# Kernel optimization log

Hardware: AMD Instinct MI355X
Metric: run time of the kernel (lower is better)

## Reference

```python
import jax, jax.numpy as jnp
import numpy as np

B, N, M, G = 2, 8192, 8192, 256
X_MIN = Y_MIN = -35.0
CELL = abs(2.0 * X_MIN / G)  # cell size, as in construct_batched_cuda_grid


def setup_inputs() -> dict:
    key = jax.random.key(0)
    k1, k2, k3, k4, k5 = jax.random.split(key, 5)
    p_i = jax.random.uniform(k1, (B, N, 3), jnp.float32, -34.0, 34.0)
    p_j = jax.random.uniform(k2, (B, M, 3), jnp.float32, -34.0, 34.0)
    mos = jax.random.normal(k3, (B, 2, G, G), jnp.float32)
    error_p_i_flow = jax.random.uniform(k4, (B, N), jnp.float32)
    nearest_flow = jax.random.randint(k5, (B, N, 1), 0, M, jnp.int32)
    return {"p_i": p_i, "mos": mos, "p_j": p_j,
            "error_p_i_flow": error_p_i_flow, "nearest_flow": nearest_flow}


def _knn1_l1(x, y):
    # brute-force 1-NN with L1 (norm=1) distance, matching knn_points(..., K=1, norm=1)
    # build (B,N,M) dist one coordinate at a time to avoid a (B,N,M,3) intermediate
    d = (jnp.abs(x[:, :, None, 0] - y[:, None, :, 0])
         + jnp.abs(x[:, :, None, 1] - y[:, None, :, 1])
         + jnp.abs(x[:, :, None, 2] - y[:, None, :, 2]))
    return jnp.min(d, axis=-1), jnp.argmin(d, axis=-1)


def reference(p_i, mos, p_j, error_p_i_flow, nearest_flow):
    # NN_loss with reduction='none' -> error_p_i_rigid = (cham_x + cham_y)/2 (needs N==M)
    cham_x, nearest_rigid = _knn1_l1(p_i, p_j)  # (B,N), (B,N)
    cham_y, _ = _knn1_l1(p_j, p_i)              # (B,M)
    error_p_i_rigid = (cham_x + cham_y) * 0.5

    dynamic = error_p_i_flow > error_p_i_rigid             # (B,N) bool
    idx = jnp.where(dynamic, nearest_flow[..., 0], nearest_rigid)  # (B,N)
    art_labels = dynamic.astype(jnp.int32)                 # (B,N) in {0,1}

    # batched gather p_j[b, idx[b]]
    p_j_by_nn = jnp.take_along_axis(p_j, idx[..., None], axis=1)  # (B,N,3)

    # construct_batched_cuda_grid: scatter labels into (B,G,G), -1 elsewhere
    shift = jnp.array([X_MIN, Y_MIN], jnp.float32)
    cell_idx = ((p_j_by_nn[:, :, :2] - shift) / CELL).astype(jnp.int32)  # (B,N,2)
    bs = jnp.repeat(jnp.arange(B), N)
    grid = -jnp.ones((B, G, G), jnp.int32)
    grid = grid.at[bs,
                   cell_idx[..., 0].reshape(-1),
                   cell_idx[..., 1].reshape(-1)].set(art_labels.reshape(-1))

    # CrossEntropyLoss(ignore_index=-1), mean over non-ignored cells
    logp = jax.nn.log_softmax(mos, axis=1)                 # (B,C,G,G)
    valid = grid >= 0
    tgt = jnp.clip(grid, 0, None)
    lp = jnp.take_along_axis(logp, tgt[:, None], axis=1)[:, 0]  # (B,G,G)
    loss = -jnp.where(valid, lp, 0.0).sum() / jnp.maximum(valid.sum(), 1).astype(lp.dtype)
    return loss
```

## Files before the change

kernel.cpp:

```cpp
#include <hip/hip_runtime.h>
#include <float.h>

#define B_ 2
#define N_ 8192
#define G_ 256
constexpr float X_MIN_F = -35.0f;
constexpr float CELL_F  = 0.2734375f;

using u64 = unsigned long long;

#define OFF_ACCUM 524288
#define OFF_PX    524352

template<int CC>
__global__ __launch_bounds__(256) void nn_kernel(const float* __restrict__ p_i,
                                                 const float* __restrict__ p_j,
                                                 u64* __restrict__ px,
                                                 float* __restrict__ colpart,
                                                 int* __restrict__ grid,
                                                 unsigned* __restrict__ accum)
{
    constexpr int COLS = N_ / CC;
    const int b    = blockIdx.z;
    const int tid  = threadIdx.x;
    const int lane = tid & 63;
    const int w    = tid >> 6;
    const int row0 = blockIdx.x * 2048 + tid * 8;
    const int c0   = blockIdx.y * COLS;

    __shared__ __align__(16) float q[COLS * 3];
    __shared__ __align__(16) float sc[4][8][36];
    __shared__ float colW[4][COLS];

    const float* __restrict__ Qg = p_j + ((size_t)b * N_ + c0) * 3;
    for (int t = tid; t < COLS * 3 / 4; t += 256)
        ((float4*)q)[t] = ((const float4*)Qg)[t];

    {
        const int lin = blockIdx.x + 4 * (blockIdx.y + CC * blockIdx.z);
        constexpr int NB  = 8 * CC;
        constexpr int PER = 32768 / NB;
        for (int t = tid; t < PER; t += 256)
            ((uint4*)grid)[lin * PER + t] = make_uint4(~0u, ~0u, ~0u, ~0u);
        if (lin == 0 && tid < 4) accum[tid] = 0u;
    }

    const float4* pp = (const float4*)(p_i + ((size_t)b * N_ + row0) * 3);
    float4 a0 = pp[0], a1 = pp[1], a2 = pp[2];
    float4 a3 = pp[3], a4 = pp[4], a5 = pp[5];
    float px_[8] = {a0.x, a0.w, a1.z, a2.y, a3.x, a3.w, a4.z, a5.y};
    float py_[8] = {a0.y, a1.x, a1.w, a2.z, a3.y, a4.x, a4.w, a5.z};
    float pz_[8] = {a0.z, a1.y, a2.x, a2.w, a3.z, a4.y, a5.x, a5.w};

    float best[8];
    int   gcol[8];
#pragma unroll
    for (int r = 0; r < 8; r++) { best[r] = FLT_MAX; gcol[r] = 0; }

    __syncthreads();

    for (int jg = 0; jg < COLS; jg += 8) {
        const float4* qv = (const float4*)&q[jg * 3];
        float4 v0 = qv[0], v1 = qv[1], v2 = qv[2];
        float4 v3 = qv[3], v4 = qv[4], v5 = qv[5];
        float qx[8] = {v0.x, v0.w, v1.z, v2.y, v3.x, v3.w, v4.z, v5.y};
        float qy[8] = {v0.y, v1.x, v1.w, v2.z, v3.y, v4.x, v4.w, v5.z};
        float qz[8] = {v0.z, v1.y, v2.x, v2.w, v3.z, v4.y, v5.x, v5.w};

        float part[8];
        {
            float dm[4][8];
#pragma unroll
            for (int r = 0; r < 4; r++) {
#pragma unroll
                for (int k = 0; k < 8; k++)
                    dm[r][k] = (fabsf(px_[r] - qx[k]) + fabsf(py_[r] - qy[k]))
                               + fabsf(pz_[r] - qz[k]);
                float m = fminf(fminf(dm[r][0], dm[r][1]), dm[r][2]);
                m = fminf(fminf(m, dm[r][3]), dm[r][4]);
                m = fminf(fminf(m, dm[r][5]), dm[r][6]);
                m = fminf(m, dm[r][7]);
                bool lt = m < best[r];
                best[r] = lt ? m : best[r];
                gcol[r] = lt ? jg : gcol[r];
            }
#pragma unroll
            for (int k = 0; k < 8; k++)
                part[k] = fminf(fminf(fminf(dm[0][k], dm[1][k]), dm[2][k]),
                                dm[3][k]);
        }
        {
            float dm[4][8];
#pragma unroll
            for (int r = 0; r < 4; r++) {
                const int rr = r + 4;
#pragma unroll
                for (int k = 0; k < 8; k++)
                    dm[r][k] = (fabsf(px_[rr] - qx[k]) + fabsf(py_[rr] - qy[k]))
                               + fabsf(pz_[rr] - qz[k]);
                float m = fminf(fminf(dm[r][0], dm[r][1]), dm[r][2]);
                m = fminf(fminf(m, dm[r][3]), dm[r][4]);
                m = fminf(fminf(m, dm[r][5]), dm[r][6]);
                m = fminf(m, dm[r][7]);
                bool lt = m < best[rr];
                best[rr] = lt ? m : best[rr];
                gcol[rr] = lt ? jg : gcol[rr];
            }
#pragma unroll
            for (int k = 0; k < 8; k++)
                part[k] = fminf(part[k],
                                fminf(fminf(fminf(dm[0][k], dm[1][k]),
                                            dm[2][k]), dm[3][k]));
        }

#pragma unroll
        for (int k = 0; k < 8; k++) {
            unsigned a = __float_as_uint(part[k]);
            auto pr = __builtin_amdgcn_permlane32_swap(a, a, false, false);
            part[k] = fminf(__uint_as_float(pr[0]), __uint_as_float(pr[1]));
        }
#pragma unroll
        for (int k = 0; k < 8; k++)
            sc[w][k][lane & 31] = part[k];
        const int kc = lane >> 3, mc = lane & 7;
        float4 c4v = *(const float4*)&sc[w][kc][4 * mc];
        float c4 = fminf(fminf(c4v.x, c4v.y), fminf(c4v.z, c4v.w));
        c4 = fminf(c4, __shfl_xor(c4, 1));
        c4 = fminf(c4, __shfl_xor(c4, 2));
        c4 = fminf(c4, __shfl_xor(c4, 4));
        if (mc == 0) colW[w][jg + kc] = c4;
    }

    __syncthreads();

    for (int t = tid; t < COLS; t += 256) {
        float c = fminf(fminf(colW[0][t], colW[1][t]),
                        fminf(colW[2][t], colW[3][t]));
        colpart[(size_t)blockIdx.x * (B_ * N_) + (size_t)b * N_ + c0 + t] = c;
    }

    int bidx[8];
#pragma unroll
    for (int r = 0; r < 8; r++) {
        const float4* qv = (const float4*)&q[gcol[r] * 3];
        float4 v0 = qv[0], v1 = qv[1], v2 = qv[2];
        float4 v3 = qv[3], v4 = qv[4], v5 = qv[5];
        float qx[8] = {v0.x, v0.w, v1.z, v2.y, v3.x, v3.w, v4.z, v5.y};
        float qy[8] = {v0.y, v1.x, v1.w, v2.z, v3.y, v4.x, v4.w, v5.z};
        float qz[8] = {v0.z, v1.y, v2.x, v2.w, v3.z, v4.y, v5.x, v5.w};
        int kk = 0;
#pragma unroll
        for (int k = 7; k >= 0; k--) {
            float d = (fabsf(px_[r] - qx[k]) + fabsf(py_[r] - qy[k]))
                      + fabsf(pz_[r] - qz[k]);
            kk = (d == best[r]) ? k : kk;
        }
        bidx[r] = c0 + gcol[r] + kk;
    }
    const size_t o = (size_t)blockIdx.y * (B_ * N_) + b * N_ + row0;
#pragma unroll
    for (int r = 0; r < 8; r++)
        px[o + r] = ((u64)__float_as_uint(best[r]) << 32) | (unsigned)bidx[r];
}

template<int CC>
__global__ __launch_bounds__(256) void reduce_scatter_kernel(
    const u64* __restrict__ px, const float* __restrict__ cp,
    const float* __restrict__ flow, const int* __restrict__ nflow,
    const float* __restrict__ Pj, int* __restrict__ grid)
{
    __shared__ u64      sbx[64];
    __shared__ unsigned sby[64];
    const int tid = threadIdx.x;
    const int p   = tid & 63;
    const int g   = tid >> 6;
    constexpr int CPG = CC / 4;

    if (tid < 64) { sbx[tid] = ~0ull; sby[tid] = ~0u; }
    __syncthreads();

    const int pt = blockIdx.x * 64 + p;
    u64 bx = ~0ull;
#pragma unroll
    for (int k = 0; k < CPG; k++) {
        int c = g * CPG + k;
        u64 v = px[(size_t)c * (B_ * N_) + pt];
        bx = v < bx ? v : bx;
    }
    float by = cp[(size_t)g * (B_ * N_) + pt];
    atomicMin(&sbx[p], bx);
    atomicMin(&sby[p], __float_as_uint(by));
    __syncthreads();

    if (tid < 64) {
        u64 fx = sbx[tid];
        float dx = __uint_as_float((unsigned)(fx >> 32));
        float dy = __uint_as_float(sby[tid]);
        float rigid = (dx + dy) * 0.5f;

        const int i = blockIdx.x * 64 + tid;
        const int b = i >> 13;
        const int n = i & (N_ - 1);

        bool dyn  = flow[i] > rigid;
        int label = dyn ? 1 : 0;
        int idx   = dyn ? nflow[i] : (int)(unsigned)(fx & 0xFFFFFFFFull);

        const float* qp = Pj + ((size_t)b * N_ + idx) * 3;
        float xx = qp[0], yy = qp[1];

        int cx = (int)((xx - X_MIN_F) / CELL_F);
        int cy = (int)((yy - X_MIN_F) / CELL_F);

        atomicMax(&grid[(b << 16) + cx * G_ + cy], (n << 1) | label);
    }
}

__global__ __launch_bounds__(256) void ce_kernel(const float* __restrict__ mos,
                                                 const int* __restrict__ grid,
                                                 float* __restrict__ accum,
                                                 float* __restrict__ out)
{
    int i = blockIdx.x * 256 + threadIdx.x;
    float lsum = 0.0f;
    int   lcnt = 0;

    int packed = grid[i];
    if (packed >= 0) {
        int b    = i >> 16;
        int cell = i & 0xFFFF;
        float m0 = mos[((size_t)b * 2 + 0) * 65536 + cell];
        float m1 = mos[((size_t)b * 2 + 1) * 65536 + cell];
        float mx = fmaxf(m0, m1);
        float lse = logf(expf(m0 - mx) + expf(m1 - mx));
        float sh  = ((packed & 1) ? m1 : m0) - mx;
        lsum = sh - lse;
        lcnt = 1;
    }

#pragma unroll
    for (int o = 32; o > 0; o >>= 1) {
        lsum += __shfl_down(lsum, o);
        lcnt += __shfl_down(lcnt, o);
    }
    __shared__ float wsum[4];
    __shared__ int   wcnt[4];
    int wave = threadIdx.x >> 6;
    if ((threadIdx.x & 63) == 0) { wsum[wave] = lsum; wcnt[wave] = lcnt; }
    __syncthreads();
    if (threadIdx.x == 0) {
        float s = wsum[0] + wsum[1] + wsum[2] + wsum[3];
        int   c = wcnt[0] + wcnt[1] + wcnt[2] + wcnt[3];
        atomicAdd(&accum[0], s);
        atomicAdd((int*)&accum[1], c);
        __threadfence();
        unsigned t = atomicAdd((unsigned*)&accum[2], 1u);
        if (t == gridDim.x - 1) {
            float S = atomicAdd(&accum[0], 0.0f);
            int   C = atomicAdd((int*)&accum[1], 0);
            out[0] = -S / (float)(C > 0 ? C : 1);
        }
    }
}

template<int CC>
static void run(const float* p_i, const float* mos, const float* p_j,
                const float* flow, const int* nflow, float* out,
                char* ws, hipStream_t stream)
{
    int*   grid    = (int*)ws;
    float* accum   = (float*)(ws + OFF_ACCUM);
    u64*   px      = (u64*)(ws + OFF_PX);
    float* colpart = (float*)(ws + OFF_PX + (size_t)CC * B_ * N_ * 8);

    dim3 g(4, CC, 2);
    nn_kernel<CC><<<g, 256, 0, stream>>>(p_i, p_j, px, colpart, (int*)grid,
                                         (unsigned*)accum);
    reduce_scatter_kernel<CC><<<256, 256, 0, stream>>>(px, colpart, flow,
                                                       nflow, p_j, grid);
    ce_kernel<<<(B_ * G_ * G_) / 256, 256, 0, stream>>>(mos, grid, accum, out);
}

extern "C" void kernel_launch(void* const* d_in, const int* in_sizes, int n_in,
                              void* d_out, int out_size, void* d_ws, size_t ws_size,
                              hipStream_t stream)
{
    const float* p_i   = (const float*)d_in[0];
    const float* mos   = (const float*)d_in[1];
    const float* p_j   = (const float*)d_in[2];
    const float* flow  = (const float*)d_in[3];
    const int*   nflow = (const int*)d_in[4];
    float* out = (float*)d_out;
    char* ws = (char*)d_ws;

    constexpr size_t CPART = (size_t)4 * B_ * N_ * 4;
    if (ws_size >= OFF_PX + (size_t)64 * B_ * N_ * 8 + CPART)
        run<64>(p_i, mos, p_j, flow, nflow, out, ws, stream);
    else if (ws_size >= OFF_PX + (size_t)16 * B_ * N_ * 8 + CPART)
        run<16>(p_i, mos, p_j, flow, nflow, out, ws, stream);
    else
        run<8>(p_i, mos, p_j, flow, nflow, out, ws, stream);
}
```

Baseline: 117.6 us.

## Write per-wave column minima to global, double-buffer LDS scratch

After: 120.0 us. 1.02x slower.

```diff
diff --git a/kernel.cpp b/kernel.cpp
--- a/kernel.cpp
+++ b/kernel.cpp
@@ -29,8 +29,7 @@
     const int c0   = blockIdx.y * COLS;
 
     __shared__ __align__(16) float q[COLS * 3];
-    __shared__ __align__(16) float sc[4][8][36];
-    __shared__ float colW[4][COLS];
+    __shared__ __align__(16) float sc[2][4][8][36];
 
     const float* __restrict__ Qg = p_j + ((size_t)b * N_ + c0) * 3;
     for (int t = tid; t < COLS * 3 / 4; t += 256)
@@ -57,9 +56,13 @@
 #pragma unroll
     for (int r = 0; r < 8; r++) { best[r] = FLT_MAX; gcol[r] = 0; }
 
+    const int kc = lane >> 3, mc = lane & 7;
+    float* cp_base = colpart + ((size_t)(blockIdx.x * 4 + w)) * (B_ * N_)
+                   + (size_t)b * N_ + c0;
+
     __syncthreads();
 
-    for (int jg = 0; jg < COLS; jg += 8) {
+    auto compute_group = [&](int jg) {
         const float4* qv = (const float4*)&q[jg * 3];
         float4 v0 = qv[0], v1 = qv[1], v2 = qv[2];
         float4 v3 = qv[3], v4 = qv[4], v5 = qv[5];
@@ -113,31 +116,31 @@
                                             dm[2][k]), dm[3][k]));
         }
 
+        float (*scb)[36] = sc[(jg >> 3) & 1][w];
 #pragma unroll
         for (int k = 0; k < 8; k++) {
             unsigned a = __float_as_uint(part[k]);
             auto pr = __builtin_amdgcn_permlane32_swap(a, a, false, false);
-            part[k] = fminf(__uint_as_float(pr[0]), __uint_as_float(pr[1]));
-        }
-#pragma unroll
-        for (int k = 0; k < 8; k++)
-            sc[w][k][lane & 31] = part[k];
-        const int kc = lane >> 3, mc = lane & 7;
-        float4 c4v = *(const float4*)&sc[w][kc][4 * mc];
+            scb[k][lane & 31] = fminf(__uint_as_float(pr[0]),
+                                      __uint_as_float(pr[1]));
+        }
+    };
+
+    auto finalize = [&](int buf, int colbase) {
+        float4 c4v = *(const float4*)&sc[buf][w][kc][4 * mc];
         float c4 = fminf(fminf(c4v.x, c4v.y), fminf(c4v.z, c4v.w));
         c4 = fminf(c4, __shfl_xor(c4, 1));
         c4 = fminf(c4, __shfl_xor(c4, 2));
         c4 = fminf(c4, __shfl_xor(c4, 4));
-        if (mc == 0) colW[w][jg + kc] = c4;
-    }
-
-    __syncthreads();
-
-    for (int t = tid; t < COLS; t += 256) {
-        float c = fminf(fminf(colW[0][t], colW[1][t]),
-                        fminf(colW[2][t], colW[3][t]));
-        colpart[(size_t)blockIdx.x * (B_ * N_) + (size_t)b * N_ + c0 + t] = c;
-    }
+        if (mc == 0) cp_base[colbase + kc] = c4;
+    };
+
+    compute_group(0);
+    for (int jg = 8; jg < COLS; jg += 8) {
+        compute_group(jg);
+        finalize(((jg >> 3) & 1) ^ 1, jg - 8);
+    }
+    finalize((COLS / 8 - 1) & 1, COLS - 8);
 
     int bidx[8];
 #pragma unroll
@@ -187,7 +190,10 @@
         u64 v = px[(size_t)c * (B_ * N_) + pt];
         bx = v < bx ? v : bx;
     }
-    float by = cp[(size_t)g * (B_ * N_) + pt];
+    float by = fminf(fminf(cp[(size_t)(g * 4 + 0) * (B_ * N_) + pt],
+                           cp[(size_t)(g * 4 + 1) * (B_ * N_) + pt]),
+                     fminf(cp[(size_t)(g * 4 + 2) * (B_ * N_) + pt],
+                           cp[(size_t)(g * 4 + 3) * (B_ * N_) + pt]));
     atomicMin(&sbx[p], bx);
     atomicMin(&sby[p], __float_as_uint(by));
     __syncthreads();
@@ -293,7 +299,7 @@
     float* out = (float*)d_out;
     char* ws = (char*)d_ws;
 
-    constexpr size_t CPART = (size_t)4 * B_ * N_ * 4;
+    constexpr size_t CPART = (size_t)16 * B_ * N_ * 4;
     if (ws_size >= OFF_PX + (size_t)64 * B_ * N_ * 8 + CPART)
         run<64>(p_i, mos, p_j, flow, nflow, out, ws, stream);
     else if (ws_size >= OFF_PX + (size_t)16 * B_ * N_ * 8 + CPART)
```
